# Kernel optimization log

Hardware: AMD Instinct MI355X
Metric: run time of the kernel (lower is better)

The kernel has to match this reference:

```python
import jax, jax.numpy as jnp
import numpy as np

B, N, F, H, D = 4096, 14, 768, 1, 768  # batch, num_diseases, feature_dim, num_heads, hidden_dim
L = 3  # number of GAT layers


def setup_inputs() -> dict:
    key = jax.random.key(0)
    ks = jax.random.split(key, 8)
    features = jax.random.normal(ks[0], (B, N, F), dtype=jnp.float32)
    # random adjacency mask; ensure nonzero diagonal so no row is fully masked
    mask = (jax.random.uniform(ks[1], (B, N, N)) > 0.3).astype(jnp.float32)
    adj = jnp.maximum(mask, jnp.eye(N, dtype=jnp.float32))
    W_emb = jax.random.normal(ks[2], (F, D), dtype=jnp.float32) / np.sqrt(F)
    b_emb = jnp.zeros((D,), dtype=jnp.float32)
    gat_W = jax.random.normal(ks[3], (L, D, H * D), dtype=jnp.float32) / np.sqrt(D)
    gat_a = jax.random.normal(ks[4], (L, 2 * D, H), dtype=jnp.float32) / np.sqrt(2 * D)
    W_out = jax.random.normal(ks[5], (H * D, F), dtype=jnp.float32) / np.sqrt(H * D)
    b_out = jnp.zeros((F,), dtype=jnp.float32)
    return dict(features=features, adj=adj, W_emb=W_emb, b_emb=b_emb,
                gat_W=gat_W, gat_a=gat_a, W_out=W_out, b_out=b_out)


def _gat_layer(x, adj, W, a):
    # x: [B, N, D], W: [D, H*D], a: [2D, H]
    Bm, Nn = x.shape[0], x.shape[1]
    Wh = (x @ W).reshape(Bm, Nn, H, D)
    # e[b,i,j,h] = Wh[b,i,h] . a[:D,h] + Wh[b,j,h] . a[D:,h]  (concat attention, un-materialized)
    a_i, a_j = a[:D], a[D:]
    ei = jnp.einsum('bnhd,dh->bnh', Wh, a_i)
    ej = jnp.einsum('bnhd,dh->bnh', Wh, a_j)
    e = ei[:, :, None, :] + ej[:, None, :, :]  # [B, N, N, H]
    e = jnp.where(adj[..., None] > 0, e, jnp.float32(-1e30))  # masked_fill(-inf)
    attn = jax.nn.softmax(e, axis=2)  # softmax over j (dim=2), matches torch
    h = jnp.einsum('bijh,bjhd->bihd', attn, Wh)  # attention-weighted aggregation
    return h.reshape(Bm, Nn, H * D), attn  # concat=True output


def reference(features, adj, W_emb, b_emb, gat_W, gat_a, W_out, b_out):
    # dropout layers are identity at inference
    x = features @ W_emb + b_emb  # disease_embedding
    attns = []
    for l in range(L):
        x, attn = _gat_layer(x, adj, gat_W[l], gat_a[l])
        attns.append(attn)
        if l < L - 1:
            x = jax.nn.elu(x)
    out = x @ W_out + b_out  # output_proj
    return (out, attns[0], attns[1], attns[2])
```

## Files before the change

### kernel.cpp

```cpp
#include <hip/hip_runtime.h>

typedef unsigned short u16;
typedef float f32x4 __attribute__((ext_vector_type(4)));
typedef float f32x16 __attribute__((ext_vector_type(16)));
typedef short bf16x8 __attribute__((ext_vector_type(8)));
typedef unsigned short u16x8 __attribute__((ext_vector_type(8)));

#define ND 768
#define KD 768

__device__ __forceinline__ float bf2f(u16 u) {
    union { unsigned i; float f; } v; v.i = ((unsigned)u) << 16; return v.f;
}
__device__ __forceinline__ u16 f2bf(float f) {
    union { float f; unsigned u; } x; x.f = f;
    unsigned r = x.u + 0x7fffu + ((x.u >> 16) & 1u);
    return (u16)(r >> 16);
}
__device__ __forceinline__ void async16(const void* g, void* l) {
    __builtin_amdgcn_global_load_lds((const __attribute__((address_space(1))) void*)g,
                                     (__attribute__((address_space(3))) void*)l, 16, 0, 0);
}

__global__ __launch_bounds__(256) void conv_w(const float* __restrict__ W_emb,
                                              const float* __restrict__ gat_W,
                                              const float* __restrict__ W_out,
                                              u16* __restrict__ Wt)
{
    __shared__ float lds[64][65];
    const int m  = blockIdx.x / 144;
    const int r  = blockIdx.x % 144;
    const int tr = r / 12;
    const int tc = r % 12;
    const float* src = (m == 0) ? W_emb : (m <= 3) ? (gat_W + (size_t)(m - 1) * 589824) : W_out;
    const int c  = threadIdx.x & 63;
    const int w4 = threadIdx.x >> 6;
    #pragma unroll
    for (int i = 0; i < 16; ++i) {
        int kk = i * 4 + w4;
        lds[kk][c] = src[(size_t)(tr * 64 + kk) * 768 + tc * 64 + c];
    }
    __syncthreads();
    u16* dst = Wt + (size_t)m * 589824;
    #pragma unroll
    for (int i = 0; i < 16; ++i) {
        int nn = i * 4 + w4;
        dst[(size_t)(tc * 64 + nn) * 768 + tr * 64 + c] = f2bf(lds[c][nn]);
    }
}

__global__ __launch_bounds__(256) void conv_x(const float4* __restrict__ in,
                                              u16* __restrict__ outp, int n4)
{
    for (int i = blockIdx.x * 256 + threadIdx.x; i < n4; i += gridDim.x * 256) {
        float4 v = in[i];
        union { u16 s[4]; uint2 u; } o;
        o.s[0] = f2bf(v.x); o.s[1] = f2bf(v.y); o.s[2] = f2bf(v.z); o.s[3] = f2bf(v.w);
        ((uint2*)outp)[i] = o.u;
    }
}

template<bool F32OUT>
__global__ __launch_bounds__(256) void gemm_bt(const u16* __restrict__ A,
                                               const u16* __restrict__ Bt,
                                               const float* __restrict__ bias,
                                               void* __restrict__ Cout)
{
    __shared__ u16 lds2[2][2][4096];
    const int tid  = threadIdx.x;
    const int lane = tid & 63;
    const int wvb  = tid & ~63;
    const int wm   = ((tid >> 7) & 1) * 64;
    const int wn   = ((tid >> 6) & 1) * 64;
    const int wg = blockIdx.x;
    const int id = (wg & 7) * 336 + (wg >> 3);
    const int tn = (id % 6) * 128;
    const int tm = (id / 6) * 128;

    f32x16 acc[2][2] = {};

    const int r31 = lane & 31;
    const int l5  = lane >> 5;
    const int key = (r31 >> 1) & 3;

    const int row0 = tid >> 2;
    const int kc0  = (((tid & 3) ^ ((tid >> 3) & 3)) << 3);
    const u16* aSrc = A  + (size_t)(tm + row0) * KD + kc0;
    const u16* bSrc = Bt + (size_t)(tn + row0) * KD + kc0;

    #define STAGE(b, ks_) { const int k0 = (ks_) * 32;                      \
        async16(aSrc + k0,                  &lds2[b][0][wvb * 8]);          \
        async16(aSrc + (size_t)64 * KD + k0, &lds2[b][0][(256 + wvb) * 8]); \
        async16(bSrc + k0,                  &lds2[b][1][wvb * 8]);          \
        async16(bSrc + (size_t)64 * KD + k0, &lds2[b][1][(256 + wvb) * 8]); }

    STAGE(0, 0);

    #pragma unroll 2
    for (int ks = 0; ks < KD / 32; ++ks) {
        const int cur = ks & 1;
        if (ks + 1 < KD / 32) {
            STAGE(cur ^ 1, ks + 1);
            asm volatile("s_waitcnt vmcnt(4)" ::: "memory");
        } else {
            asm volatile("s_waitcnt vmcnt(0)" ::: "memory");
        }
        __builtin_amdgcn_s_barrier();
        asm volatile("" ::: "memory");

        const u16* As = lds2[cur][0];
        const u16* Bs = lds2[cur][1];
        bf16x8 af[2][2], bf[2][2];
        #pragma unroll
        for (int fr = 0; fr < 2; ++fr)
            #pragma unroll
            for (int ka = 0; ka < 2; ++ka) {
                int chA = ((ka * 2 + l5) ^ key) << 3;
                af[fr][ka] = *(const bf16x8*)&As[(wm + fr * 32 + r31) * 32 + chA];
                bf[fr][ka] = *(const bf16x8*)&Bs[(wn + fr * 32 + r31) * 32 + chA];
            }
        #pragma unroll
        for (int fr = 0; fr < 2; ++fr)
            #pragma unroll
            for (int fc = 0; fc < 2; ++fc)
                #pragma unroll
                for (int ka = 0; ka < 2; ++ka)
                    acc[fr][fc] = __builtin_amdgcn_mfma_f32_32x32x16_bf16(
                        af[fr][ka], bf[fc][ka], acc[fr][fc], 0, 0, 0);

        if (ks + 1 < KD / 32) {
            asm volatile("" ::: "memory");
            __builtin_amdgcn_s_barrier();
        }
    }
    #undef STAGE

    #pragma unroll
    for (int fc = 0; fc < 2; ++fc) {
        int col = tn + wn + fc * 32 + r31;
        float bv = bias ? bias[col] : 0.0f;
        #pragma unroll
        for (int fr = 0; fr < 2; ++fr) {
            int rowb = tm + wm + fr * 32 + 4 * l5;
            #pragma unroll
            for (int reg = 0; reg < 16; ++reg) {
                int row = rowb + (reg & 3) + 8 * (reg >> 2);
                float v = acc[fr][fc][reg] + bv;
                if (F32OUT)
                    ((float*)Cout)[(size_t)row * ND + col] = v;
                else
                    ((u16*)Cout)[(size_t)row * ND + col] = f2bf(v);
            }
        }
    }
}

template<bool ELU>
__global__ __launch_bounds__(256) void gat_mix(const u16* __restrict__ Wh,
                                               const float* __restrict__ adj,
                                               const float* __restrict__ avec,
                                               float* __restrict__ attn_out,
                                               u16* __restrict__ Xout)
{
    __shared__ u16 wh[14 * 768];
    __shared__ float s_ei[14], s_ej[14];
    __shared__ float s_attn[196];
    const int b = blockIdx.x;
    const int tid = threadIdx.x;
    const u16* whb = Wh + (size_t)b * 10752;

    for (int c = tid; c < 1344; c += 256)
        ((uint4*)wh)[c] = ((const uint4*)whb)[c];
    __syncthreads();

    if (tid < 224) {
        const int i = tid >> 4, l = tid & 15;
        float ai = 0.f, aj = 0.f;
        #pragma unroll
        for (int c = 0; c < 6; ++c) {
            int d = c * 128 + l * 8;
            u16x8 v  = *(const u16x8*)&wh[i * 768 + d];
            float4 x0 = *(const float4*)&avec[d];
            float4 x1 = *(const float4*)&avec[d + 4];
            float4 y0 = *(const float4*)&avec[768 + d];
            float4 y1 = *(const float4*)&avec[768 + d + 4];
            float w0 = bf2f(v[0]), w1 = bf2f(v[1]), w2 = bf2f(v[2]), w3 = bf2f(v[3]);
            float w4 = bf2f(v[4]), w5 = bf2f(v[5]), w6 = bf2f(v[6]), w7 = bf2f(v[7]);
            ai += w0*x0.x + w1*x0.y + w2*x0.z + w3*x0.w + w4*x1.x + w5*x1.y + w6*x1.z + w7*x1.w;
            aj += w0*y0.x + w1*y0.y + w2*y0.z + w3*y0.w + w4*y1.x + w5*y1.y + w6*y1.z + w7*y1.w;
        }
        #pragma unroll
        for (int off = 8; off; off >>= 1) {
            ai += __shfl_xor(ai, off);
            aj += __shfl_xor(aj, off);
        }
        if (l == 0) { s_ei[i] = ai; s_ej[i] = aj; }
    }
    __syncthreads();

    if (tid < 14) {
        const int i = tid;
        float e[14];
        float mx = -3.0e38f;
        #pragma unroll
        for (int j = 0; j < 14; ++j) {
            float ev = (adj[(size_t)b * 196 + i * 14 + j] > 0.f) ? (s_ei[i] + s_ej[j]) : -1.0e30f;
            e[j] = ev; mx = fmaxf(mx, ev);
        }
        float sum = 0.f;
        #pragma unroll
        for (int j = 0; j < 14; ++j) { float pp = __expf(e[j] - mx); e[j] = pp; sum += pp; }
        float inv = 1.0f / sum;
        #pragma unroll
        for (int j = 0; j < 14; ++j) s_attn[i * 14 + j] = e[j] * inv;
    }
    __syncthreads();

    if (tid < 196) attn_out[(size_t)b * 196 + tid] = s_attn[tid];

    for (int pp = tid; pp < 14 * 48; pp += 256) {
        const int i  = pp / 48;
        const int d0 = (pp % 48) * 16;
        float acc[16] = {};
        #pragma unroll
        for (int j = 0; j < 14; ++j) {
            float aw = s_attn[i * 14 + j];
            u16x8 wv0 = *(const u16x8*)&wh[j * 768 + d0];
            u16x8 wv1 = *(const u16x8*)&wh[j * 768 + d0 + 8];
            #pragma unroll
            for (int qq = 0; qq < 8; ++qq) {
                acc[qq]     += aw * bf2f(wv0[qq]);
                acc[8 + qq] += aw * bf2f(wv1[qq]);
            }
        }
        union { u16 s[16]; uint4 u[2]; } o;
        #pragma unroll
        for (int qq = 0; qq < 16; ++qq) {
            float v = acc[qq];
            if (ELU && v < 0.f) v = __expf(v) - 1.0f;
            o.s[qq] = f2bf(v);
        }
        *(uint4*)&Xout[(size_t)b * 10752 + i * 768 + d0]     = o.u[0];
        *(uint4*)&Xout[(size_t)b * 10752 + i * 768 + d0 + 8] = o.u[1];
    }
}

extern "C" void kernel_launch(void* const* d_in, const int* in_sizes, int n_in,
                              void* d_out, int out_size, void* d_ws, size_t ws_size,
                              hipStream_t stream)
{
    const float* features = (const float*)d_in[0];
    const float* adj      = (const float*)d_in[1];
    const float* W_emb    = (const float*)d_in[2];
    const float* b_emb    = (const float*)d_in[3];
    const float* gat_W    = (const float*)d_in[4];
    const float* gat_a    = (const float*)d_in[5];
    const float* W_out    = (const float*)d_in[6];
    const float* b_out    = (const float*)d_in[7];
    float* out = (float*)d_out;

    u16* Wh = (u16*)d_ws;
    u16* Wt = Wh + 44040192;
    u16* H0 = (u16*)d_out;
    u16* H1 = H0 + 44040192;
    float* attn0 = out + 44040192;
    float* attn1 = attn0 + 802816;
    float* attn2 = attn1 + 802816;

    conv_w<<<dim3(720), 256, 0, stream>>>(W_emb, gat_W, W_out, Wt);
    conv_x<<<dim3(4096), 256, 0, stream>>>((const float4*)features, H0, 11010048);

    dim3 gg(2688);
    gemm_bt<false><<<gg, 256, 0, stream>>>(H0, Wt, b_emb, H1);
    gemm_bt<false><<<gg, 256, 0, stream>>>(H1, Wt + 589824, nullptr, Wh);
    gat_mix<true><<<dim3(4096), 256, 0, stream>>>(Wh, adj, gat_a, attn0, H0);
    gemm_bt<false><<<gg, 256, 0, stream>>>(H0, Wt + 2 * 589824, nullptr, Wh);
    gat_mix<true><<<dim3(4096), 256, 0, stream>>>(Wh, adj, gat_a + 1536, attn1, H1);
    gemm_bt<false><<<gg, 256, 0, stream>>>(H1, Wt + 3 * 589824, nullptr, Wh);
    gat_mix<false><<<dim3(4096), 256, 0, stream>>>(Wh, adj, gat_a + 3072, attn2, Wh);
    gemm_bt<true><<<gg, 256, 0, stream>>>(Wh, Wt + 4 * 589824, b_out, (void*)out);
}
```

Baseline: 707.7 us.

## Fold embedding and final projection weights into adjacent GAT GEMMs

Precomputes the products W_emb·W1 and W3·W_out on device so the chain has two fewer large GEMMs. Layer-3 attention logits are derived from layer-2 output through precomputed vectors W3·a, and the last layer aggregates over the already-projected values, writing fp32 output plus bias. This relies on attention mixing commuting with the right-side linear map. In exchange it adds small setup kernels and atomics in gat_mix, and the fused weights are rounded to bf16, which changes numerics.

```diff
diff --git a/kernel.cpp b/kernel.cpp
--- a/kernel.cpp
+++ b/kernel.cpp
@@ -49,6 +49,28 @@
     }
 }
 
+__global__ __launch_bounds__(256) void conv_w1(const float* __restrict__ src,
+                                               u16* __restrict__ dst)
+{
+    __shared__ float lds[64][65];
+    const int r  = blockIdx.x;
+    const int tr = r / 12;
+    const int tc = r % 12;
+    const int c  = threadIdx.x & 63;
+    const int w4 = threadIdx.x >> 6;
+    #pragma unroll
+    for (int i = 0; i < 16; ++i) {
+        int kk = i * 4 + w4;
+        lds[kk][c] = src[(size_t)(tr * 64 + kk) * 768 + tc * 64 + c];
+    }
+    __syncthreads();
+    #pragma unroll
+    for (int i = 0; i < 16; ++i) {
+        int nn = i * 4 + w4;
+        dst[(size_t)(tc * 64 + nn) * 768 + tr * 64 + c] = f2bf(lds[c][nn]);
+    }
+}
+
 __global__ __launch_bounds__(256) void conv_x(const float4* __restrict__ in,
                                               u16* __restrict__ outp, int n4)
 {
@@ -60,7 +82,27 @@
     }
 }
 
-template<bool F32OUT>
+__global__ __launch_bounds__(256) void prep_vecs(const float* __restrict__ W3,
+                                                 const float* __restrict__ ga2,
+                                                 const float* __restrict__ be,
+                                                 const u16* __restrict__ Wt1,
+                                                 float* __restrict__ w3ai,
+                                                 float* __restrict__ w3aj,
+                                                 float* __restrict__ bfus)
+{
+    int d = blockIdx.x * 256 + threadIdx.x;
+    if (d >= 768) return;
+    const float* row = W3 + (size_t)d * 768;
+    float ai = 0.f, aj = 0.f;
+    for (int n = 0; n < 768; ++n) { float w = row[n]; ai += w * ga2[n]; aj += w * ga2[768 + n]; }
+    w3ai[d] = ai; w3aj[d] = aj;
+    const u16* wt = Wt1 + (size_t)d * 768;
+    float bf = 0.f;
+    for (int j = 0; j < 768; ++j) bf += be[j] * bf2f(wt[j]);
+    bfus[d] = bf;
+}
+
+template<bool F32OUT, bool SWZ>
 __global__ __launch_bounds__(256) void gemm_bt(const u16* __restrict__ A,
                                                const u16* __restrict__ Bt,
                                                const float* __restrict__ bias,
@@ -73,7 +115,7 @@
     const int wm   = ((tid >> 7) & 1) * 64;
     const int wn   = ((tid >> 6) & 1) * 64;
     const int wg = blockIdx.x;
-    const int id = (wg & 7) * 336 + (wg >> 3);
+    const int id = SWZ ? ((wg & 7) * 336 + (wg >> 3)) : wg;
     const int tn = (id % 6) * 128;
     const int tm = (id / 6) * 128;
 
@@ -155,20 +197,26 @@
     }
 }
 
-template<bool ELU>
+template<bool ELU, bool DOTS>
 __global__ __launch_bounds__(256) void gat_mix(const u16* __restrict__ Wh,
                                                const float* __restrict__ adj,
                                                const float* __restrict__ avec,
                                                float* __restrict__ attn_out,
-                                               u16* __restrict__ Xout)
+                                               u16* __restrict__ Xout,
+                                               const float* __restrict__ w3ai,
+                                               const float* __restrict__ w3aj,
+                                               float* __restrict__ eiOut,
+                                               float* __restrict__ ejOut)
 {
     __shared__ u16 wh[14 * 768];
     __shared__ float s_ei[14], s_ej[14];
     __shared__ float s_attn[196];
+    __shared__ float s_dots[14][2];
     const int b = blockIdx.x;
     const int tid = threadIdx.x;
     const u16* whb = Wh + (size_t)b * 10752;
 
+    if (DOTS && tid < 28) ((float*)s_dots)[tid] = 0.f;
     for (int c = tid; c < 1344; c += 256)
         ((uint4*)wh)[c] = ((const uint4*)whb)[c];
     __syncthreads();
@@ -233,15 +281,92 @@
                 acc[8 + qq] += aw * bf2f(wv1[qq]);
             }
         }
+        float pi = 0.f, pj = 0.f;
         union { u16 s[16]; uint4 u[2]; } o;
         #pragma unroll
         for (int qq = 0; qq < 16; ++qq) {
             float v = acc[qq];
             if (ELU && v < 0.f) v = __expf(v) - 1.0f;
+            if (DOTS) { pi += v * w3ai[d0 + qq]; pj += v * w3aj[d0 + qq]; }
             o.s[qq] = f2bf(v);
+        }
+        if (DOTS) {
+            atomicAdd(&s_dots[i][0], pi);
+            atomicAdd(&s_dots[i][1], pj);
         }
         *(uint4*)&Xout[(size_t)b * 10752 + i * 768 + d0]     = o.u[0];
         *(uint4*)&Xout[(size_t)b * 10752 + i * 768 + d0 + 8] = o.u[1];
+    }
+    if (DOTS) {
+        __syncthreads();
+        if (tid < 14) {
+            eiOut[(size_t)b * 14 + tid] = s_dots[tid][0];
+            ejOut[(size_t)b * 14 + tid] = s_dots[tid][1];
+        }
+    }
+}
+
+__global__ __launch_bounds__(256) void gat_out(const u16* __restrict__ Z,
+                                               const float* __restrict__ adj,
+                                               const float* __restrict__ eiG,
+                                               const float* __restrict__ ejG,
+                                               const float* __restrict__ b_out,
+                                               float* __restrict__ attn_out,
+                                               float* __restrict__ outp)
+{
+    __shared__ u16 wh[14 * 768];
+    __shared__ float s_attn[196];
+    const int b = blockIdx.x;
+    const int tid = threadIdx.x;
+    const u16* zb = Z + (size_t)b * 10752;
+
+    for (int c = tid; c < 1344; c += 256)
+        ((uint4*)wh)[c] = ((const uint4*)zb)[c];
+
+    if (tid < 14) {
+        const int i = tid;
+        float ei = eiG[(size_t)b * 14 + i];
+        float e[14];
+        float mx = -3.0e38f;
+        #pragma unroll
+        for (int j = 0; j < 14; ++j) {
+            float ev = (adj[(size_t)b * 196 + i * 14 + j] > 0.f)
+                           ? (ei + ejG[(size_t)b * 14 + j]) : -1.0e30f;
+            e[j] = ev; mx = fmaxf(mx, ev);
+        }
+        float sum = 0.f;
+        #pragma unroll
+        for (int j = 0; j < 14; ++j) { float pp = __expf(e[j] - mx); e[j] = pp; sum += pp; }
+        float inv = 1.0f / sum;
+        #pragma unroll
+        for (int j = 0; j < 14; ++j) s_attn[i * 14 + j] = e[j] * inv;
+    }
+    __syncthreads();
+
+    if (tid < 196) attn_out[(size_t)b * 196 + tid] = s_attn[tid];
+
+    for (int pp = tid; pp < 14 * 48; pp += 256) {
+        const int i  = pp / 48;
+        const int d0 = (pp % 48) * 16;
+        float acc[16];
+        #pragma unroll
+        for (int qq = 0; qq < 16; ++qq) acc[qq] = b_out[d0 + qq];
+        #pragma unroll
+        for (int j = 0; j < 14; ++j) {
+            float aw = s_attn[i * 14 + j];
+            u16x8 wv0 = *(const u16x8*)&wh[j * 768 + d0];
+            u16x8 wv1 = *(const u16x8*)&wh[j * 768 + d0 + 8];
+            #pragma unroll
+            for (int qq = 0; qq < 8; ++qq) {
+                acc[qq]     += aw * bf2f(wv0[qq]);
+                acc[8 + qq] += aw * bf2f(wv1[qq]);
+            }
+        }
+        float* dst = &outp[(size_t)b * 10752 + i * 768 + d0];
+        *(float4*)(dst)      = *(float4*)&acc[0];
+        *(float4*)(dst + 4)  = *(float4*)&acc[4];
+        *(float4*)(dst + 8)  = *(float4*)&acc[8];
+        *(float4*)(dst + 12) = *(float4*)&acc[12];
     }
 }
 
@@ -261,22 +386,38 @@
 
     u16* Wh = (u16*)d_ws;
     u16* Wt = Wh + 44040192;
+    float* scr  = (float*)(Wt + 7 * 589824);
+    float* w3ai = scr + 589824;
+    float* w3aj = w3ai + 768;
+    float* bfus = w3aj + 768;
+    float* eiG  = bfus + 768;
+    float* ejG  = eiG + 57344;
     u16* H0 = (u16*)d_out;
     u16* H1 = H0 + 44040192;
+    u16* WeBf = H1;
+    u16* W3Bf = H1 + 589824;
     float* attn0 = out + 44040192;
     float* attn1 = attn0 + 802816;
     float* attn2 = attn1 + 802816;
 
     conv_w<<<dim3(720), 256, 0, stream>>>(W_emb, gat_W, W_out, Wt);
     conv_x<<<dim3(4096), 256, 0, stream>>>((const float4*)features, H0, 11010048);
+    conv_x<<<dim3(576), 256, 0, stream>>>((const float4*)W_emb, WeBf, 147456);
+    conv_x<<<dim3(576), 256, 0, stream>>>((const float4*)(gat_W + 2 * 589824), W3Bf, 147456);
+    prep_vecs<<<dim3(3), 256, 0, stream>>>(gat_W + 2 * 589824, gat_a + 2 * 1536, b_emb,
+                                           Wt + 589824, w3ai, w3aj, bfus);
+    gemm_bt<true, false><<<dim3(36), 256, 0, stream>>>(WeBf, Wt + 1 * 589824, nullptr, scr);
+    conv_w1<<<dim3(144), 256, 0, stream>>>(scr, Wt + 5 * 589824);
+    gemm_bt<true, false><<<dim3(36), 256, 0, stream>>>(W3Bf, Wt + 4 * 589824, nullptr, scr);
+    conv_w1<<<dim3(144), 256, 0, stream>>>(scr, Wt + 6 * 589824);
 
     dim3 gg(2688);
-    gemm_bt<false><<<gg, 256, 0, stream>>>(H0, Wt, b_emb, H1);
-    gemm_bt<false><<<gg, 256, 0, stream>>>(H1, Wt + 589824, nullptr, Wh);
-    gat_mix<true><<<dim3(4096), 256, 0, stream>>>(Wh, adj, gat_a, attn0, H0);
-    gemm_bt<false><<<gg, 256, 0, stream>>>(H0, Wt + 2 * 589824, nullptr, Wh);
-    gat_mix<true><<<dim3(4096), 256, 0, stream>>>(Wh, adj, gat_a + 1536, attn1, H1);
-    gemm_bt<false><<<gg, 256, 0, stream>>>(H1, Wt + 3 * 589824, nullptr, Wh);
-    gat_mix<false><<<dim3(4096), 256, 0, stream>>>(Wh, adj, gat_a + 3072, attn2, Wh);
-    gemm_bt<true><<<gg, 256, 0, stream>>>(Wh, Wt + 4 * 589824, b_out, (void*)out);
-}
+    gemm_bt<false, true><<<gg, 256, 0, stream>>>(H0, Wt + 5 * 589824, bfus, Wh);
+    gat_mix<true, false><<<dim3(4096), 256, 0, stream>>>(Wh, adj, gat_a, attn0, H1,
+                                                         nullptr, nullptr, nullptr, nullptr);
+    gemm_bt<false, true><<<gg, 256, 0, stream>>>(H1, Wt + 2 * 589824, nullptr, Wh);
+    gat_mix<true, true><<<dim3(4096), 256, 0, stream>>>(Wh, adj, gat_a + 1536, attn1, H0,
+                                                        w3ai, w3aj, eiG, ejG);
+    gemm_bt<false, true><<<gg, 256, 0, stream>>>(H0, Wt + 6 * 589824, nullptr, Wh);
+    gat_out<<<dim3(4096), 256, 0, stream>>>(Wh, adj, eiG, ejG, b_out, attn2, out);
+}
```

Result: faster. 661.7 us (-6.5%).
